# Optimization experiments

Measured on AMD Instinct MI355X. Metric: run time of the kernel, lower is better.

Reference implementation:

```python
import jax, jax.numpy as jnp
import numpy as np

# Normalizer hyperparameters (from init_kwargs)
THETA = 0.3     # final temperature theta
THETA0 = 4.0    # initial annealing temperature
T = 20          # number of annealing iterations
BETA = 0.7      # temperature decay
P = 0.1         # fraction -> k = p * (# finite entries per row)
TEMPERATURE = 1.0

BSZ, SEQ = 4096, 8192


def setup_inputs() -> dict:
    key = jax.random.key(0)
    k1, k2 = jax.random.split(key)
    score = jax.random.normal(k1, (BSZ, SEQ), dtype=jnp.float32)
    mask = jax.random.randint(k2, (BSZ, SEQ), 0, 2, dtype=jnp.int32)
    return {"score": score, "mask": mask}


def reference(score, mask):
    # score: [bsz, seq], mask: [bsz, seq] (0 = masked out)
    score = score * TEMPERATURE
    score = jnp.where(mask == 0, -jnp.inf, score)

    # k = p * number of finite (unmasked) entries per row
    k = jnp.sum(jnp.isfinite(score), axis=-1, keepdims=True).astype(score.dtype) * P

    # annealed temperature schedule: theta_t = max(beta^t * theta0, theta)
    thetas = [max(BETA ** t * THETA0, THETA) for t in range(T)]

    a = jnp.zeros((score.shape[0], 1), dtype=score.dtype)
    b = jnp.zeros_like(score)
    for th in thetas:
        # masked entries: exp(-inf)=0, relu(-inf)=0 -> they contribute nothing
        s = jnp.sum(jnp.exp((score + b) / th), axis=-1, keepdims=True)  # [bsz,1]
        a = th * jnp.log(k / (s + 1e-20))                               # [bsz,1]
        b = -jax.nn.relu(score + a)                                     # [bsz,seq]

    gamma = jnp.exp((score + a + b) / THETA)  # [bsz, seq]
    return gamma
```

## Files before the change

kernel.cpp:

```cpp
#include <hip/hip_runtime.h>
#include <math.h>

#define SEQ      8192
#define NTHREADS 256
#define VPT      32
#define F4PT     8

__device__ __forceinline__ float wave_sum(float x) {
    #pragma unroll
    for (int off = 32; off > 0; off >>= 1)
        x += __shfl_xor(x, off, 64);
    return x;
}

__global__ __launch_bounds__(NTHREADS, 8) void normalizer_kernel(
        const float* __restrict__ score,
        const int*   __restrict__ mask,
        float*       __restrict__ out)
{
    const int row  = blockIdx.x;
    const int tid  = threadIdx.x;
    const int wid  = tid >> 6;
    const int lane = tid & 63;

    constexpr double L2E = 1.4426950408889634;
    constexpr double TH7 = 4.0*0.7*0.7*0.7*0.7*0.7*0.7*0.7;
    const float cu0 = (float)(L2E / 4.0);
    const float r07 = (float)(1.0 / 0.7);
    const float ce  = (float)(TH7 / 0.3);

    const float4* __restrict__ s4 = (const float4*)(score + (size_t)row * SEQ);
    const int4*   __restrict__ m4 = (const int4*)(mask  + (size_t)row * SEQ);

    float u[VPT];
    int cnt = 0;
    #pragma unroll
    for (int j = 0; j < F4PT; ++j) {
        float4 s = s4[j * NTHREADS + tid];
        int4   m = m4[j * NTHREADS + tid];
        u[4*j+0] = m.x ? s.x * cu0 : -INFINITY;
        u[4*j+1] = m.y ? s.y * cu0 : -INFINITY;
        u[4*j+2] = m.z ? s.z * cu0 : -INFINITY;
        u[4*j+3] = m.w ? s.w * cu0 : -INFINITY;
        cnt += (m.x != 0) + (m.y != 0) + (m.z != 0) + (m.w != 0);
    }

    __shared__ float redc[4];
    __shared__ float red[2][4];

    float a0 = 0.f, a1 = 0.f;
    #pragma unroll
    for (int j = 0; j < VPT; j += 2) {
        a0 += __builtin_amdgcn_exp2f(u[j]);
        a1 += __builtin_amdgcn_exp2f(u[j+1]);
    }
    float pc = wave_sum((float)cnt);
    float ps = wave_sum(a0 + a1);
    if (lane == 0) { redc[wid] = pc; red[0][wid] = ps; }
    #pragma unroll
    for (int j = 0; j < VPT; ++j) u[j] *= r07;
    __syncthreads();
    const float k   = 0.1f * (redc[0] + redc[1] + redc[2] + redc[3]);
    const float l2k = __builtin_amdgcn_logf(k);
    const float rk  = 1.0f / k;
    float s_ = red[0][0] + red[0][1] + red[0][2] + red[0][3];
    float NAcp = (__builtin_amdgcn_logf(s_ + 1e-20f) - l2k) * r07;

    for (int t = 1; t < 7; ++t) {
        a0 = 0.f; a1 = 0.f;
        #pragma unroll
        for (int j = 0; j < VPT; j += 2) {
            a0 += __builtin_amdgcn_exp2f(fminf(u[j],   NAcp));
            a1 += __builtin_amdgcn_exp2f(fminf(u[j+1], NAcp));
        }
        float pa = wave_sum(a0 + a1);
        if (lane == 0) red[t & 1][wid] = pa;
        #pragma unroll
        for (int j = 0; j < VPT; ++j) u[j] *= r07;
        __syncthreads();
        s_ = red[t & 1][0] + red[t & 1][1] + red[t & 1][2] + red[t & 1][3];
        NAcp = (__builtin_amdgcn_logf(s_ + 1e-20f) - l2k) * r07;
    }

    {
        a0 = 0.f; a1 = 0.f;
        #pragma unroll
        for (int j = 0; j < VPT; j += 2) {
            a0 += __builtin_amdgcn_exp2f(fminf(u[j],   NAcp));
            a1 += __builtin_amdgcn_exp2f(fminf(u[j+1], NAcp));
        }
        float pa = wave_sum(a0 + a1);
        if (lane == 0) red[1][wid] = pa;
        #pragma unroll
        for (int j = 0; j < VPT; ++j)
            u[j] = __builtin_amdgcn_exp2f(u[j] * ce);
        __syncthreads();
        s_ = red[1][0] + red[1][1] + red[1][2] + red[1][3];
    }
    float eNA = __builtin_amdgcn_exp2f((__builtin_amdgcn_logf(s_ + 1e-20f) - l2k) * ce);

    for (int t = 8; t < 20; ++t) {
        a0 = 0.f; a1 = 0.f;
        #pragma unroll
        for (int j = 0; j < VPT; j += 2) {
            a0 += fminf(u[j],   eNA);
            a1 += fminf(u[j+1], eNA);
        }
        float pa = wave_sum(a0 + a1);
        if (lane == 0) red[t & 1][wid] = pa;
        __syncthreads();
        s_ = red[t & 1][0] + red[t & 1][1] + red[t & 1][2] + red[t & 1][3];
        eNA = (s_ + 1e-20f) * rk;
    }

    const float ra = 1.0f / eNA;
    float4* __restrict__ o4 = (float4*)(out + (size_t)row * SEQ);
    #pragma unroll
    for (int j = 0; j < F4PT; ++j) {
        float4 g;
        g.x = fminf(u[4*j+0], eNA) * ra;
        g.y = fminf(u[4*j+1], eNA) * ra;
        g.z = fminf(u[4*j+2], eNA) * ra;
        g.w = fminf(u[4*j+3], eNA) * ra;
        o4[j * NTHREADS + tid] = g;
    }
}

extern "C" void kernel_launch(void* const* d_in, const int* in_sizes, int n_in,
                              void* d_out, int out_size, void* d_ws, size_t ws_size,
                              hipStream_t stream) {
    const float* score = (const float*)d_in[0];
    const int*   mask  = (const int*)d_in[1];
    float*       out   = (float*)d_out;
    const int rows = in_sizes[0] / SEQ;
    normalizer_kernel<<<rows, NTHREADS, 0, stream>>>(score, mask, out);
}
```

Measured before the change: 329.6 us.

## Process each row with a single wavefront to remove block barriers

Each row is now handled by one 64-lane wavefront holding 128 values per lane in registers, instead of four waves with 32 values each. All 20 per-iteration reductions become pure wave shuffles, with no shared memory or __syncthreads. The accumulation uses four independent chains instead of two. In exchange, register pressure rises sharply (128 live floats per lane), which lowers occupancy and may cause spills, and memory latency hiding now relies on fewer waves per CU.

```diff
diff --git a/kernel.cpp b/kernel.cpp
--- a/kernel.cpp
+++ b/kernel.cpp
@@ -1,10 +1,10 @@
 #include <hip/hip_runtime.h>
 #include <math.h>
 
-#define SEQ      8192
-#define NTHREADS 256
-#define VPT      32
-#define F4PT     8
+#define SEQ   8192
+#define NT    64
+#define VPT   128
+#define F4PT  32
 
 __device__ __forceinline__ float wave_sum(float x) {
     #pragma unroll
@@ -13,15 +13,13 @@
     return x;
 }
 
-__global__ __launch_bounds__(NTHREADS, 8) void normalizer_kernel(
+__global__ __launch_bounds__(NT) void normalizer_kernel(
         const float* __restrict__ score,
         const int*   __restrict__ mask,
         float*       __restrict__ out)
 {
     const int row  = blockIdx.x;
-    const int tid  = threadIdx.x;
-    const int wid  = tid >> 6;
-    const int lane = tid & 63;
+    const int lane = threadIdx.x;
 
     constexpr double L2E = 1.4426950408889634;
     constexpr double TH7 = 4.0*0.7*0.7*0.7*0.7*0.7*0.7*0.7;
@@ -36,8 +34,8 @@
     int cnt = 0;
     #pragma unroll
     for (int j = 0; j < F4PT; ++j) {
-        float4 s = s4[j * NTHREADS + tid];
-        int4   m = m4[j * NTHREADS + tid];
+        float4 s = s4[j * NT + lane];
+        int4   m = m4[j * NT + lane];
         u[4*j+0] = m.x ? s.x * cu0 : -INFINITY;
         u[4*j+1] = m.y ? s.y * cu0 : -INFINITY;
         u[4*j+2] = m.z ? s.z * cu0 : -INFINITY;
@@ -45,72 +43,65 @@
         cnt += (m.x != 0) + (m.y != 0) + (m.z != 0) + (m.w != 0);
     }
 
-    __shared__ float redc[4];
-    __shared__ float red[2][4];
-
-    float a0 = 0.f, a1 = 0.f;
+    float a0 = 0.f, a1 = 0.f, a2 = 0.f, a3 = 0.f;
     #pragma unroll
-    for (int j = 0; j < VPT; j += 2) {
+    for (int j = 0; j < VPT; j += 4) {
         a0 += __builtin_amdgcn_exp2f(u[j]);
         a1 += __builtin_amdgcn_exp2f(u[j+1]);
+        a2 += __builtin_amdgcn_exp2f(u[j+2]);
+        a3 += __builtin_amdgcn_exp2f(u[j+3]);
     }
-    float pc = wave_sum((float)cnt);
-    float ps = wave_sum(a0 + a1);
-    if (lane == 0) { redc[wid] = pc; red[0][wid] = ps; }
+    float s_ = wave_sum((a0 + a1) + (a2 + a3));
+    float kf = 0.1f * wave_sum((float)cnt);
     #pragma unroll
     for (int j = 0; j < VPT; ++j) u[j] *= r07;
-    __syncthreads();
-    const float k   = 0.1f * (redc[0] + redc[1] + redc[2] + redc[3]);
-    const float l2k = __builtin_amdgcn_logf(k);
-    const float rk  = 1.0f / k;
-    float s_ = red[0][0] + red[0][1] + red[0][2] + red[0][3];
+    const float l2k = __builtin_amdgcn_logf(kf);
+    const float rk  = 1.0f / kf;
     float NAcp = (__builtin_amdgcn_logf(s_ + 1e-20f) - l2k) * r07;
 
     for (int t = 1; t < 7; ++t) {
-        a0 = 0.f; a1 = 0.f;
+        a0 = 0.f; a1 = 0.f; a2 = 0.f; a3 = 0.f;
         #pragma unroll
-        for (int j = 0; j < VPT; j += 2) {
+        for (int j = 0; j < VPT; j += 4) {
             a0 += __builtin_amdgcn_exp2f(fminf(u[j],   NAcp));
             a1 += __builtin_amdgcn_exp2f(fminf(u[j+1], NAcp));
+            a2 += __builtin_amdgcn_exp2f(fminf(u[j+2], NAcp));
+            a3 += __builtin_amdgcn_exp2f(fminf(u[j+3], NAcp));
         }
-        float pa = wave_sum(a0 + a1);
-        if (lane == 0) red[t & 1][wid] = pa;
         #pragma unroll
         for (int j = 0; j < VPT; ++j) u[j] *= r07;
-        __syncthreads();
-        s_ = red[t & 1][0] + red[t & 1][1] + red[t & 1][2] + red[t & 1][3];
-        NAcp = (__builtin_amdgcn_logf(s_ + 1e-20f) - l2k) * r07;
+        float ss = wave_sum((a0 + a1) + (a2 + a3));
+        NAcp = (__builtin_amdgcn_logf(ss + 1e-20f) - l2k) * r07;
     }
 
+    float eNA;
     {
-        a0 = 0.f; a1 = 0.f;
+        a0 = 0.f; a1 = 0.f; a2 = 0.f; a3 = 0.f;
         #pragma unroll
-        for (int j = 0; j < VPT; j += 2) {
+        for (int j = 0; j < VPT; j += 4) {
             a0 += __builtin_amdgcn_exp2f(fminf(u[j],   NAcp));
             a1 += __builtin_amdgcn_exp2f(fminf(u[j+1], NAcp));
+            a2 += __builtin_amdgcn_exp2f(fminf(u[j+2], NAcp));
+            a3 += __builtin_amdgcn_exp2f(fminf(u[j+3], NAcp));
         }
-        float pa = wave_sum(a0 + a1);
-        if (lane == 0) red[1][wid] = pa;
         #pragma unroll
         for (int j = 0; j < VPT; ++j)
             u[j] = __builtin_amdgcn_exp2f(u[j] * ce);
-        __syncthreads();
-        s_ = red[1][0] + red[1][1] + red[1][2] + red[1][3];
+        float ss = wave_sum((a0 + a1) + (a2 + a3));
+        eNA = __builtin_amdgcn_exp2f((__builtin_amdgcn_logf(ss + 1e-20f) - l2k) * ce);
     }
-    float eNA = __builtin_amdgcn_exp2f((__builtin_amdgcn_logf(s_ + 1e-20f) - l2k) * ce);
 
     for (int t = 8; t < 20; ++t) {
-        a0 = 0.f; a1 = 0.f;
+        a0 = 0.f; a1 = 0.f; a2 = 0.f; a3 = 0.f;
         #pragma unroll
-        for (int j = 0; j < VPT; j += 2) {
+        for (int j = 0; j < VPT; j += 4) {
             a0 += fminf(u[j],   eNA);
             a1 += fminf(u[j+1], eNA);
+            a2 += fminf(u[j+2], eNA);
+            a3 += fminf(u[j+3], eNA);
         }
-        float pa = wave_sum(a0 + a1);
-        if (lane == 0) red[t & 1][wid] = pa;
-        __syncthreads();
-        s_ = red[t & 1][0] + red[t & 1][1] + red[t & 1][2] + red[t & 1][3];
-        eNA = (s_ + 1e-20f) * rk;
+        float ss = wave_sum((a0 + a1) + (a2 + a3));
+        eNA = (ss + 1e-20f) * rk;
     }
 
     const float ra = 1.0f / eNA;
@@ -122,7 +113,7 @@
         g.y = fminf(u[4*j+1], eNA) * ra;
         g.z = fminf(u[4*j+2], eNA) * ra;
         g.w = fminf(u[4*j+3], eNA) * ra;
-        o4[j * NTHREADS + tid] = g;
+        o4[j * NT + lane] = g;
     }
 }
 
@@ -133,5 +124,5 @@
     const int*   mask  = (const int*)d_in[1];
     float*       out   = (float*)d_out;
     const int rows = in_sizes[0] / SEQ;
-    normalizer_kernel<<<rows, NTHREADS, 0, stream>>>(score, mask, out);
+    normalizer_kernel<<<rows, NT, 0, stream>>>(score, mask, out);
 }
```

After: 367.7 us. +11.6%, slower.
